# Kernel optimization log

Hardware: AMD Instinct MI355X
Metric: run time of the kernel (lower is better)

The kernel has to match this reference:

```python
import jax, jax.numpy as jnp
import numpy as np
from jax import lax

B, X, H, W, C = 4, 32, 8, 128, 32  # batch, frames, height, width, channels (dim)


def setup_inputs() -> dict:
    key = jax.random.key(0)
    k1, k2, k3, k4, k5, k6 = jax.random.split(key, 6)
    return {
        "storage": jax.random.normal(k1, (B, X, H, W, C), jnp.float32),
        "target": jax.random.normal(k2, (B, 1, H, W, C), jnp.float32),
        # Conv3d(dim, 2*dim, kernel=(3,1,1), padding=(1,0,0)) weight/bias
        "w_cross": jax.random.normal(k3, (2 * C, C, 3, 1, 1), jnp.float32) * 0.05,
        "b_cross": jax.random.normal(k4, (2 * C,), jnp.float32) * 0.05,
        # Conv2d(dim, dim, kernel=1) weight (stored as [out, in]) / bias
        "w_q": jax.random.normal(k5, (C, C), jnp.float32) * 0.1,
        "b_q": jax.random.normal(k6, (C,), jnp.float32) * 0.1,
    }


def reference(storage, target, w_cross, b_cross, w_q, b_q):
    # storage [B,X,H,W,C] -> transpose(4,1).transpose(4,2) -> [B,C,X,W,H]
    s = jnp.transpose(storage, (0, 4, 1, 3, 2))
    # target [B,1,H,W,C] -> transpose(4,2) -> [B,1,C,W,H] -> squeeze(1) -> [B,C,W,H]
    t = jnp.transpose(target, (0, 1, 4, 3, 2))[:, 0]

    # Conv3d over the X (depth) axis, kernel (3,1,1), padding (1,0,0)
    out = lax.conv_general_dilated(
        s, w_cross, window_strides=(1, 1, 1),
        padding=((1, 1), (0, 0), (0, 0)),
        dimension_numbers=("NCDHW", "OIDHW", "NCDHW"),
    ) + b_cross[None, :, None, None, None]          # [B,2C,X,W,H]
    s_v, s_k = jnp.split(out, 2, axis=1)            # each [B,C,X,W,H]

    # 1x1 Conv2d query projection
    t_q = jnp.einsum("oc,bcwh->bowh", w_q, t) + b_q[None, :, None, None]  # [B,C,W,H]
    # unsqueeze(1).transpose(2,1).repeat over X -> [B,C,X,W,H]
    t_q = jnp.broadcast_to(t_q[:, :, None], (B, C, X, W, H))

    # Faithful torch .view on contiguous [B,C,X,W,H]: row-major reshape mixes C into last dim
    t_q = t_q.reshape(B, X * W, C * H)
    s_v = s_v.reshape(B, X * W, C * H)
    s_k = jnp.swapaxes(s_k.reshape(B, X * W, C * H), 1, 2)  # [B, C*H, X*W]

    kq = jax.nn.softmax(jnp.einsum("bnc,bcm->bnm", t_q, s_k), axis=-1)  # [B, XW, XW]
    final = jnp.einsum("bnm,bmc->bnc", kq, s_v)                          # [B, XW, C*H]
    return final.reshape(B, X, H, W, C)
```

## Files before the change

### kernel.cpp

```cpp
#include <hip/hip_runtime.h>

typedef unsigned short u16;
typedef unsigned int u32;
typedef __attribute__((ext_vector_type(8))) short s16x8;
typedef __attribute__((ext_vector_type(4))) float f32x4;

#define WS_A      0u
#define WS_B      8388608u
#define WS_C      16777216u
#define WS_LP     25452544u
#define WS_NEEDED 25485312u

__device__ __forceinline__ u16 f2bf(float f){
  u32 u = __float_as_uint(f);
  return (u16)((u + 0x7fffu + ((u >> 16) & 1u)) >> 16);
}

__global__ __launch_bounds__(256) void zero_out_kernel(float* __restrict__ out){
  int t = blockIdx.x * 256 + threadIdx.x;
  ((float4*)out)[t] = make_float4(0.f, 0.f, 0.f, 0.f);
}

__global__ __launch_bounds__(512, 4) void conv_kernel(const float* __restrict__ storage,
    const float* __restrict__ w_cross, const float* __restrict__ b_cross,
    u16* __restrict__ Kb, u16* __restrict__ Vb){
  __shared__ alignas(16) char smem[65536];
  u16* Hp0 = (u16*)smem;
  u16* Lp0 = (u16*)(smem + 16384);
  u16* Hp1 = (u16*)(smem + 32768);
  u16* Lp1 = (u16*)(smem + 49152);

  int o_idx = (blockIdx.x & 7) * 64 + (blockIdx.x >> 3);
  int wc = o_idx & 3;
  int x  = (o_idx >> 2) & 31;
  int b  = o_idx >> 7;
  int tid = threadIdx.x;
  int w8 = tid >> 6;
  int oh = w8 >> 1, mh = w8 & 1;
  int lane = tid & 63, l15 = lane & 15, quad = lane >> 4;

  s16x8 Ahi[3], Alo[3];
  {
    int o = oh*16 + l15;
    const float4* wp = (const float4*)(w_cross + o*96 + quad*24);
    float w24[24];
    #pragma unroll
    for (int i = 0; i < 6; ++i){
      float4 v = wp[i];
      w24[i*4+0] = v.x; w24[i*4+1] = v.y; w24[i*4+2] = v.z; w24[i*4+3] = v.w;
    }
    #pragma unroll
    for (int dx = 0; dx < 3; ++dx){
      #pragma unroll
      for (int e = 0; e < 8; ++e){
        float wv = w24[e*3 + dx];
        u32 u = __float_as_uint(wv);
        float r = wv - __uint_as_float(u & 0xffff0000u);
        Ahi[dx][e] = (short)(u >> 16);
        Alo[dx][e] = (short)(__float_as_uint(r) >> 16);
      }
    }
  }

  f32x4 acc[8];
  {
    float4 bv = *(const float4*)(b_cross + oh*16 + quad*4);
    #pragma unroll
    for (int mt = 0; mt < 8; ++mt) acc[mt] = (f32x4){bv.x, bv.y, bv.z, bv.w};
  }

  auto STAGE = [&](int dx, u16* H, u16* L){
    int xx = x + dx - 1;
    const float* src = storage + (size_t)(b*32 + xx)*32768;
    #pragma unroll
    for (int r = 0; r < 4; ++r){
      int e = r*2048 + tid*4;
      int h = e >> 10, w = (e >> 5) & 31, c = e & 31;
      float4 v = *(const float4*)(src + h*4096 + (wc*32 + w)*32 + c);
      int idx = (h*32 + w)*32 + (((c >> 3) ^ (h & 3)) << 3) + (c & 7);
      float f[4] = {v.x, v.y, v.z, v.w};
      ushort4 hv, lv;
      u16* hp = (u16*)&hv; u16* lp = (u16*)&lv;
      #pragma unroll
      for (int k2 = 0; k2 < 4; ++k2){
        u32 u = __float_as_uint(f[k2]);
        float rr = f[k2] - __uint_as_float(u & 0xffff0000u);
        hp[k2] = (u16)(u >> 16);
        lp[k2] = (u16)(__float_as_uint(rr) >> 16);
      }
      *(ushort4*)&H[idx] = hv;
      *(ushort4*)&L[idx] = lv;
    }
  };

  auto CONSUME = [&](s16x8 ah, s16x8 al, const u16* H, const u16* L){
    int h = l15 & 7;
    int cb = quad ^ (h & 3);
    #pragma unroll
    for (int mt = 0; mt < 8; ++mt){
      int wr = mh*16 + mt*2 + (l15 >> 3);
      int idx = (h*32 + wr)*32 + cb*8;
      s16x8 bhi = *(const s16x8*)&H[idx];
      s16x8 blo = *(const s16x8*)&L[idx];
      acc[mt] = __builtin_amdgcn_mfma_f32_16x16x32_bf16(ah, bhi, acc[mt], 0, 0, 0);
      acc[mt] = __builtin_amdgcn_mfma_f32_16x16x32_bf16(ah, blo, acc[mt], 0, 0, 0);
      acc[mt] = __builtin_amdgcn_mfma_f32_16x16x32_bf16(al, bhi, acc[mt], 0, 0, 0);
    }
  };

  bool has0 = (x > 0), has2 = (x < 31);
  if (has0) STAGE(0, Hp0, Lp0); else STAGE(1, Hp1, Lp1);
  __syncthreads();
  if (has0){
    STAGE(1, Hp1, Lp1);
    CONSUME(Ahi[0], Alo[0], Hp0, Lp0);
    __syncthreads();
  }
  {
    if (has2) STAGE(2, Hp0, Lp0);
    CONSUME(Ahi[1], Alo[1], Hp1, Lp1);
    __syncthreads();
  }
  if (has2){
    CONSUME(Ahi[2], Alo[2], Hp0, Lp0);
    __syncthreads();
  }

  u16* st = (u16*)smem;
  #pragma unroll
  for (int mt = 0; mt < 8; ++mt){
    #pragma unroll
    for (int r = 0; r < 4; ++r)
      st[(oh*16 + quad*4 + r)*264 + mh*128 + mt*16 + l15] = f2bf(acc[mt][r]);
  }
  __syncthreads();
  int o_loc = tid >> 3, part = tid & 7;
  size_t base = ((size_t)b*4096 + (size_t)(o_loc & 31)*128 + (size_t)x*4 + wc)*256 + part*8;
  u16* dst = (o_loc < 32 ? Vb : Kb) + base;
  const u16* srcp = &st[o_loc*264 + part*8];
  #pragma unroll
  for (int i = 0; i < 4; ++i)
    *(uint4*)(dst + i*64) = *(const uint4*)(srcp + i*64);
}

__global__ __launch_bounds__(256, 2) void flash_kernel(const float* __restrict__ target,
    const float* __restrict__ w_q, const float* __restrict__ b_q,
    const u16* __restrict__ Kb, const u16* __restrict__ Vb,
    float* __restrict__ Opart, float* __restrict__ lpart){
  int kq = blockIdx.x & 15, rb = (blockIdx.x >> 4) & 7, b = blockIdx.x >> 7;
  int tid = threadIdx.x;
  int w = tid >> 6, lane = tid & 63, l15 = lane & 15, quad = lane >> 4;

  __shared__ alignas(16) u16 Vts[256 * 64];
  __shared__ alignas(16) u16 Ps[16 * 64];
  __shared__ float lsumW[64];

  u16* stgQ = Vts;
  {
    int wl = tid & 31, h = tid >> 5;
    #pragma unroll
    for (int wcq = 0; wcq < 4; ++wcq){
      float in[32];
      const float4* p = (const float4*)(target + (((size_t)b*8 + h)*128 + wcq*32 + wl)*32);
      #pragma unroll
      for (int q = 0; q < 8; ++q){
        float4 v = p[q];
        in[q*4+0] = v.x; in[q*4+1] = v.y; in[q*4+2] = v.z; in[q*4+3] = v.w;
      }
      #pragma unroll
      for (int cql = 0; cql < 4; ++cql){
        int cq = rb*4 + cql;
        float acc = b_q[cq];
        #pragma unroll
        for (int c = 0; c < 32; ++c) acc = fmaf(in[c], w_q[cq*32 + c], acc);
        stgQ[(cql*4 + wcq)*264 + wl*8 + h] = f2bf(acc);
      }
    }
  }
  __syncthreads();

  s16x8 qa[8];
  {
    const u16* qp = stgQ + l15*264 + quad*8;
    #pragma unroll
    for (int ks = 0; ks < 8; ++ks) qa[ks] = *(const s16x8*)(qp + ks*32);
  }
  __syncthreads();

  int jl4 = tid & 15, mseg = tid >> 4;
  const u16* kbase = Kb + ((size_t)(b*4096 + kq*256 + w*16 + l15))*256 + quad*8;
  const u16* vbase = Vb + ((size_t)(b*4096 + kq*256 + jl4*4))*256 + mseg*16;

  s16x8 kr[8];
  #pragma unroll
  for (int ks = 0; ks < 8; ++ks) kr[ks] = *(const s16x8*)(kbase + ks*32);
  u32 kv[4][8];
  #pragma unroll
  for (int kk = 0; kk < 4; ++kk){
    uint4 a = *(const uint4*)(vbase + kk*256);
    uint4 b2 = *(const uint4*)(vbase + kk*256 + 8);
    kv[kk][0]=a.x; kv[kk][1]=a.y; kv[kk][2]=a.z; kv[kk][3]=a.w;
    kv[kk][4]=b2.x; kv[kk][5]=b2.y; kv[kk][6]=b2.z; kv[kk][7]=b2.w;
  }

  float lacc[4] = {0.f, 0.f, 0.f, 0.f};
  f32x4 oc[4];
  #pragma unroll
  for (int mt = 0; mt < 4; ++mt) oc[mt] = (f32x4){0.f,0.f,0.f,0.f};

  #pragma unroll
  for (int it = 0; it < 4; ++it){
    if (it > 0) __syncthreads();

    #pragma unroll
    for (int i = 0; i < 16; ++i){
      int d = i >> 1;
      u32 e0, e1, e2, e3;
      if (i & 1){ e0 = kv[0][d] >> 16;     e1 = kv[1][d] >> 16;
                  e2 = kv[2][d] >> 16;     e3 = kv[3][d] >> 16; }
      else      { e0 = kv[0][d] & 0xffffu; e1 = kv[1][d] & 0xffffu;
                  e2 = kv[2][d] & 0xffffu; e3 = kv[3][d] & 0xffffu; }
      int m = mseg*16 + i;
      int col = (((jl4 >> 1) ^ (m & 7)) << 3) + ((jl4 & 1) << 2);
      *(uint2*)&Vts[m*64 + col] = make_uint2(e0 | (e1 << 16), e2 | (e3 << 16));
    }

    f32x4 s0 = {0.f,0.f,0.f,0.f}, s1 = {0.f,0.f,0.f,0.f};
    #pragma unroll
    for (int ks = 0; ks < 8; ks += 2){
      s0 = __builtin_amdgcn_mfma_f32_16x16x32_bf16(qa[ks],   kr[ks],   s0, 0, 0, 0);
      s1 = __builtin_amdgcn_mfma_f32_16x16x32_bf16(qa[ks+1], kr[ks+1], s1, 0, 0, 0);
    }
    int b8k = w*2 + (l15 >> 3);
    #pragma unroll
    for (int reg = 0; reg < 4; ++reg){
      float sv = fminf(s0[reg] + s1[reg], 80.f);
      float p = __expf(sv);
      int row = quad*4 + reg;
      Ps[row*64 + ((b8k ^ (row & 7)) << 3) + (l15 & 7)] = f2bf(p);
      lacc[reg] += p;
    }

    if (it < 3){
      const u16* vp = vbase + (it+1)*16384;
      #pragma unroll
      for (int kk = 0; kk < 4; ++kk){
        uint4 a = *(const uint4*)(vp + kk*256);
        uint4 b2 = *(const uint4*)(vp + kk*256 + 8);
        kv[kk][0]=a.x; kv[kk][1]=a.y; kv[kk][2]=a.z; kv[kk][3]=a.w;
        kv[kk][4]=b2.x; kv[kk][5]=b2.y; kv[kk][6]=b2.z; kv[kk][7]=b2.w;
      }
    }
    __syncthreads();

    if (it < 3){
      const u16* kp = kbase + (it+1)*16384;
      #pragma unroll
      for (int ks = 0; ks < 8; ++ks) kr[ks] = *(const s16x8*)(kp + ks*32);
    }
    #pragma unroll
    for (int ks2 = 0; ks2 < 2; ++ks2){
      int b8 = ks2*4 + quad;
      s16x8 pb = *(const s16x8*)&Ps[l15*64 + ((b8 ^ (l15 & 7)) << 3)];
      #pragma unroll
      for (int mt = 0; mt < 4; ++mt){
        int mrow = (w*4 + mt)*16 + l15;
        s16x8 af = *(const s16x8*)&Vts[mrow*64 + ((b8 ^ (mrow & 7)) << 3)];
        oc[mt] = __builtin_amdgcn_mfma_f32_16x16x32_bf16(af, pb, oc[mt], 0, 0, 0);
      }
    }
  }

  #pragma unroll
  for (int reg = 0; reg < 4; ++reg){
    float t = lacc[reg];
    t += __shfl_xor(t, 1); t += __shfl_xor(t, 2);
    t += __shfl_xor(t, 4); t += __shfl_xor(t, 8);
    lacc[reg] = t;
  }
  if (l15 == 0){
    #pragma unroll
    for (int reg = 0; reg < 4; ++reg) lsumW[w*16 + quad*4 + reg] = lacc[reg];
  }
  __syncthreads();
  if (tid < 16)
    lpart[(b*16 + kq)*128 + rb*16 + tid] =
        lsumW[tid] + lsumW[16 + tid] + lsumW[32 + tid] + lsumW[48 + tid];
  {
    float* dst = Opart + ((size_t)((b*16 + kq)*128 + rb*16 + l15))*256 + w*64 + quad*4;
    #pragma unroll
    for (int mt = 0; mt < 4; ++mt)
      *(float4*)(dst + mt*16) = make_float4(oc[mt][0], oc[mt][1], oc[mt][2], oc[mt][3]);
  }
}

__global__ __launch_bounds__(256) void combine_kernel(const float* __restrict__ lpart,
    const float* __restrict__ Opart, float* __restrict__ out){
  int r = blockIdx.x & 127, b = blockIdx.x >> 7;
  int m = threadIdx.x;
  float L = 0.f, o = 0.f;
  #pragma unroll
  for (int kq = 0; kq < 16; ++kq){
    L += lpart[(b*16 + kq)*128 + r];
    o += Opart[((size_t)((b*16 + kq)*128 + r))*256 + m];
  }
  o /= L;
  int cq = r >> 2, whi = r & 3;
  size_t obase = ((size_t)b*32 + cq) * 32768;
  #pragma unroll
  for (int hh = 0; hh < 8; ++hh){
    #pragma unroll
    for (int wt = 0; wt < 4; ++wt){
      out[obase + hh*4096 + wt*1024 + whi*256 + m] = o;
    }
  }
}

extern "C" void kernel_launch(void* const* d_in, const int* in_sizes, int n_in,
                              void* d_out, int out_size, void* d_ws, size_t ws_size,
                              hipStream_t stream){
  const float* storage = (const float*)d_in[0];
  const float* target  = (const float*)d_in[1];
  const float* w_cross = (const float*)d_in[2];
  const float* b_cross = (const float*)d_in[3];
  const float* w_q     = (const float*)d_in[4];
  const float* b_q     = (const float*)d_in[5];
  float* out = (float*)d_out;

  if (ws_size < (size_t)WS_NEEDED){
    zero_out_kernel<<<dim3(4096), dim3(256), 0, stream>>>(out);
    return;
  }

  char* ws = (char*)d_ws;
  float* Opart = (float*)(ws + WS_A);
  u16*   Kb    = (u16*)(ws + WS_B);
  u16*   Vb    = (u16*)(ws + WS_C);
  float* lpart = (float*)(ws + WS_LP);

  conv_kernel    <<<dim3(512), dim3(512), 0, stream>>>(storage, w_cross, b_cross, Kb, Vb);
  flash_kernel   <<<dim3(512), dim3(256), 0, stream>>>(target, w_q, b_q, Kb, Vb, Opart, lpart);
  combine_kernel <<<dim3(512), dim3(256), 0, stream>>>(lpart, Opart, out);
}
```

Measured before the change: 122.0 us.

## Split conv kernel into smaller 256-thread blocks over half-width tiles

The conv kernel now launches 1024 blocks of 256 threads, each covering 16 of the 32 W positions in its tile, instead of 512 blocks of 512 threads. Shared memory per block halves, which should raise occupancy and spread the work across more CUs. The x-1 and x slices are now both staged before the first barrier, changing the prior overlap of staging and MFMA consumption. The cost is that each block loads the weights redundantly, and the K/V stores become two narrower writes per thread.

```diff
diff --git a/kernel.cpp b/kernel.cpp
--- a/kernel.cpp
+++ b/kernel.cpp
@@ -21,27 +21,27 @@
   ((float4*)out)[t] = make_float4(0.f, 0.f, 0.f, 0.f);
 }
 
-__global__ __launch_bounds__(512, 4) void conv_kernel(const float* __restrict__ storage,
+__global__ __launch_bounds__(256, 4) void conv_kernel(const float* __restrict__ storage,
     const float* __restrict__ w_cross, const float* __restrict__ b_cross,
     u16* __restrict__ Kb, u16* __restrict__ Vb){
-  __shared__ alignas(16) char smem[65536];
-  u16* Hp0 = (u16*)smem;
-  u16* Lp0 = (u16*)(smem + 16384);
-  u16* Hp1 = (u16*)(smem + 32768);
-  u16* Lp1 = (u16*)(smem + 49152);
-
-  int o_idx = (blockIdx.x & 7) * 64 + (blockIdx.x >> 3);
-  int wc = o_idx & 3;
-  int x  = (o_idx >> 2) & 31;
-  int b  = o_idx >> 7;
+  __shared__ alignas(16) char smem[32768];
+  u16* B0H = (u16*)smem;
+  u16* B0L = B0H + 4096;
+  u16* B1H = (u16*)(smem + 16384);
+  u16* B1L = B1H + 4096;
+
+  int o_idx = (blockIdx.x & 7) * 128 + (blockIdx.x >> 3);
+  int mh = o_idx & 1;
+  int wc = (o_idx >> 1) & 3;
+  int x  = (o_idx >> 3) & 31;
+  int b  = o_idx >> 8;
   int tid = threadIdx.x;
-  int w8 = tid >> 6;
-  int oh = w8 >> 1, mh = w8 & 1;
+  int w4 = tid >> 6;
   int lane = tid & 63, l15 = lane & 15, quad = lane >> 4;
 
   s16x8 Ahi[3], Alo[3];
   {
-    int o = oh*16 + l15;
+    int o = w4*16 + l15;
     const float4* wp = (const float4*)(w_cross + o*96 + quad*24);
     float w24[24];
     #pragma unroll
@@ -64,20 +64,20 @@
 
   f32x4 acc[8];
   {
-    float4 bv = *(const float4*)(b_cross + oh*16 + quad*4);
+    float4 bv = *(const float4*)(b_cross + w4*16 + quad*4);
     #pragma unroll
     for (int mt = 0; mt < 8; ++mt) acc[mt] = (f32x4){bv.x, bv.y, bv.z, bv.w};
   }
 
-  auto STAGE = [&](int dx, u16* H, u16* L){
-    int xx = x + dx - 1;
-    const float* src = storage + (size_t)(b*32 + xx)*32768;
+  auto STAGE = [&](int xx, u16* H, u16* L){
+    const float* src = storage + ((size_t)(b*32 + xx)*8)*4096
+                       + (wc*32 + mh*16)*32;
     #pragma unroll
     for (int r = 0; r < 4; ++r){
-      int e = r*2048 + tid*4;
-      int h = e >> 10, w = (e >> 5) & 31, c = e & 31;
-      float4 v = *(const float4*)(src + h*4096 + (wc*32 + w)*32 + c);
-      int idx = (h*32 + w)*32 + (((c >> 3) ^ (h & 3)) << 3) + (c & 7);
+      int e = r*1024 + tid*4;
+      int h = e >> 9, wl16 = (e >> 5) & 15, c = e & 31;
+      float4 v = *(const float4*)(src + h*4096 + wl16*32 + c);
+      int idx = (h*16 + wl16)*32 + (((c >> 3) ^ (h & 3)) << 3) + (c & 7);
       float f[4] = {v.x, v.y, v.z, v.w};
       ushort4 hv, lv;
       u16* hp = (u16*)&hv; u16* lp = (u16*)&lv;
@@ -98,8 +98,8 @@
     int cb = quad ^ (h & 3);
     #pragma unroll
     for (int mt = 0; mt < 8; ++mt){
-      int wr = mh*16 + mt*2 + (l15 >> 3);
-      int idx = (h*32 + wr)*32 + cb*8;
+      int wl16 = mt*2 + (l15 >> 3);
+      int idx = (h*16 + wl16)*32 + cb*8;
       s16x8 bhi = *(const s16x8*)&H[idx];
       s16x8 blo = *(const s16x8*)&L[idx];
       acc[mt] = __builtin_amdgcn_mfma_f32_16x16x32_bf16(ah, bhi, acc[mt], 0, 0, 0);
@@ -109,38 +109,36 @@
   };
 
   bool has0 = (x > 0), has2 = (x < 31);
-  if (has0) STAGE(0, Hp0, Lp0); else STAGE(1, Hp1, Lp1);
-  __syncthreads();
-  if (has0){
-    STAGE(1, Hp1, Lp1);
-    CONSUME(Ahi[0], Alo[0], Hp0, Lp0);
-    __syncthreads();
-  }
-  {
-    if (has2) STAGE(2, Hp0, Lp0);
-    CONSUME(Ahi[1], Alo[1], Hp1, Lp1);
-    __syncthreads();
-  }
-  if (has2){
-    CONSUME(Ahi[2], Alo[2], Hp0, Lp0);
-    __syncthreads();
-  }
+  if (has0) STAGE(x - 1, B0H, B0L);
+  STAGE(x, B1H, B1L);
+  __syncthreads();
+  if (has0) CONSUME(Ahi[0], Alo[0], B0H, B0L);
+  __syncthreads();
+  if (has2) STAGE(x + 1, B0H, B0L);
+  CONSUME(Ahi[1], Alo[1], B1H, B1L);
+  __syncthreads();
+  if (has2) CONSUME(Ahi[2], Alo[2], B0H, B0L);
+  __syncthreads();
 
   u16* st = (u16*)smem;
   #pragma unroll
   for (int mt = 0; mt < 8; ++mt){
     #pragma unroll
     for (int r = 0; r < 4; ++r)
-      st[(oh*16 + quad*4 + r)*264 + mh*128 + mt*16 + l15] = f2bf(acc[mt][r]);
-  }
-  __syncthreads();
-  int o_loc = tid >> 3, part = tid & 7;
-  size_t base = ((size_t)b*4096 + (size_t)(o_loc & 31)*128 + (size_t)x*4 + wc)*256 + part*8;
-  u16* dst = (o_loc < 32 ? Vb : Kb) + base;
-  const u16* srcp = &st[o_loc*264 + part*8];
-  #pragma unroll
-  for (int i = 0; i < 4; ++i)
-    *(uint4*)(dst + i*64) = *(const uint4*)(srcp + i*64);
+      st[(w4*16 + quad*4 + r)*136 + mt*16 + l15] = f2bf(acc[mt][r]);
+  }
+  __syncthreads();
+  int part8 = tid & 7;
+  #pragma unroll
+  for (int p = 0; p < 2; ++p){
+    int row = p*32 + (tid >> 3);
+    size_t base = ((size_t)b*4096 + (size_t)(row & 31)*128 + (size_t)x*4 + wc)*256
+                  + mh*128 + part8*16;
+    u16* dst = (row < 32 ? Vb : Kb) + base;
+    const u16* srcp = &st[row*136 + part8*16];
+    *(uint4*)dst       = *(const uint4*)srcp;
+    *(uint4*)(dst + 8) = *(const uint4*)(srcp + 8);
+  }
 }
 
 __global__ __launch_bounds__(256, 2) void flash_kernel(const float* __restrict__ target,
@@ -338,7 +336,7 @@
   u16*   Vb    = (u16*)(ws + WS_C);
   float* lpart = (float*)(ws + WS_LP);
 
-  conv_kernel    <<<dim3(512), dim3(512), 0, stream>>>(storage, w_cross, b_cross, Kb, Vb);
-  flash_kernel   <<<dim3(512), dim3(256), 0, stream>>>(target, w_q, b_q, Kb, Vb, Opart, lpart);
-  combine_kernel <<<dim3(512), dim3(256), 0, stream>>>(lpart, Opart, out);
-}
+  conv_kernel    <<<dim3(1024), dim3(256), 0, stream>>>(storage, w_cross, b_cross, Kb, Vb);
+  flash_kernel   <<<dim3(512),  dim3(256), 0, stream>>>(target, w_q, b_q, Kb, Vb, Opart, lpart);
+  combine_kernel <<<dim3(512),  dim3(256), 0, stream>>>(lpart, Opart, out);
+}
```

New measurement: 119.3 us. -2.3%, faster.
